# Kernel optimization log

Hardware: AMD Instinct MI355X
Metric: run time of the kernel (lower is better)

## Reference

```python
import jax, jax.numpy as jnp
import numpy as np
import math

B, T, D, H, E = 4, 2048, 1024, 4096, 8
CAPACITY_FACTOR = 1.0
MIN_CAPACITY = 4
Z_LOSS_COEF = 0.001
AUX_LOSS_COEF = 0.01


def setup_inputs() -> dict:
    key = jax.random.key(0)
    ks = jax.random.split(key, 5)
    x = jax.random.normal(ks[0], (B, T, D), jnp.float32)
    Wg = jax.random.normal(ks[1], (D, E), jnp.float32) * 0.02
    W1 = jax.random.normal(ks[2], (E, D, H), jnp.float32) * (1.0 / math.sqrt(D))
    b1 = jnp.zeros((E, H), jnp.float32)
    W2 = jax.random.normal(ks[3], (E, H, D), jnp.float32) * (1.0 / math.sqrt(H))
    b2 = jnp.zeros((E, D), jnp.float32)
    return {"x": x, "Wg": Wg, "W1": W1, "b1": b1, "W2": W2, "b2": b2}


def reference(x, Wg, W1, b1, W2, b2):
    b, t, d = x.shape
    e = Wg.shape[1]
    N = b * t
    capacity = max(MIN_CAPACITY, math.ceil(CAPACITY_FACTOR * N / e))  # static
    xf = x.reshape(N, d)

    # ---- Router (top-1, z-loss + aux load-balancing loss) ----
    logits = xf @ Wg                                   # [N, E]
    probs = jax.nn.softmax(logits, axis=-1)
    z_loss = jnp.mean(jax.nn.logsumexp(logits, axis=-1) ** 2)
    expert_index = jnp.argmax(logits, axis=-1)         # [N]
    expert_prob = jnp.take_along_axis(probs, expert_index[:, None], axis=1)[:, 0]
    counts = jax.ops.segment_sum(jnp.ones((N,), jnp.float32), expert_index,
                                 num_segments=e)       # bincount
    f_i = counts / N
    p_i = probs.mean(axis=0)
    aux_loss = AUX_LOSS_COEF * e * jnp.sum(f_i * p_i) + Z_LOSS_COEF * z_loss

    # ---- Sort-based dispatch ----
    sort_idx = jnp.argsort(expert_index)               # stable sort by expert
    se = expert_index[sort_idx]                        # sorted expert ids
    xs = xf[sort_idx]                                  # tokens in sorted order
    ps = expert_prob[sort_idx]                         # probs in sorted order
    counts_i = counts.astype(jnp.int32)
    start = jnp.cumsum(counts_i) - counts_i            # per-expert start offsets
    pos = jnp.arange(N, dtype=jnp.int32) - start[se]   # slot within expert
    keep = pos < capacity                              # capacity drop
    slot = jnp.where(keep, pos, capacity)              # overflow -> trash slot

    # Gather tokens into per-expert capacity buffer [E, capacity+1, D]
    buf = jnp.zeros((e, capacity + 1, d), xf.dtype).at[se, slot].set(xs)

    # ---- Batched per-expert MLP (grouped GEMM) ----
    h = jax.nn.gelu(jnp.einsum('ecd,edh->ech', buf, W1) + b1[:, None, :],
                    approximate=False)
    o = jnp.einsum('ech,ehd->ecd', h, W2) + b2[:, None, :]

    # ---- Combine: gather back, zero dropped tokens, unsort ----
    out_sorted = jnp.where(keep[:, None], o[se, slot], jnp.zeros((), o.dtype))
    out = jnp.zeros_like(xf).at[sort_idx].set(out_sorted)
    # NOTE: faithful to original code, which multiplies the UNSORTED output by
    # the SORTED probabilities (prob_sorted), a quirk of the source module.
    out = out * ps[:, None]
    return out.reshape(b, t, d), aux_loss
```

## Files before the change

kernel.cpp:

```cpp
#include <hip/hip_runtime.h>
#include <math.h>

#define N_TOK 8192
#define DIM   1024
#define NEXP  8
#define HID   4096
#define CAP   1024
#define TPT   (N_TOK / 256)
#define RT_BLOCKS 256
#define RT_TPB (N_TOK / RT_BLOCKS)

typedef _Float16 f16x8 __attribute__((ext_vector_type(8)));
typedef _Float16 f16x4 __attribute__((ext_vector_type(4)));
typedef float    f32x4 __attribute__((ext_vector_type(4)));

__device__ __forceinline__ float gelu_exact(float v) {
    return 0.5f * v * (1.0f + erff(v * 0.7071067811865476f));
}

__device__ __forceinline__ void gl_lds16(const void* g, void* l) {
    __builtin_amdgcn_global_load_lds(
        (const __attribute__((address_space(1))) unsigned int*)g,
        (__attribute__((address_space(3))) unsigned int*)l, 16, 0, 0);
}

__global__ __launch_bounds__(256) void router_kernel(
    const float* __restrict__ x, const float* __restrict__ Wg,
    int* __restrict__ ei, float* __restrict__ eprob,
    float* __restrict__ pp)
{
    __shared__ float psum_s[NEXP + 1];
    const int tid = threadIdx.x;
    const int w = tid >> 6, lane = tid & 63;
    if (tid <= NEXP) psum_s[tid] = 0.f;
    __syncthreads();

    float p_loc[NEXP];
#pragma unroll
    for (int e = 0; e < NEXP; ++e) p_loc[e] = 0.f;
    float z_loc = 0.f;

    for (int ti = 0; ti < RT_TPB / 4; ++ti) {
        const int t = blockIdx.x * RT_TPB + w * (RT_TPB / 4) + ti;
        const float* xr = x + (size_t)t * DIM;
        float acc[NEXP];
#pragma unroll
        for (int e = 0; e < NEXP; ++e) acc[e] = 0.f;
#pragma unroll
        for (int k = 0; k < DIM / 64; ++k) {
            const int d = k * 64 + lane;
            const float xv = xr[d];
            const float4 w0 = *(const float4*)(Wg + (size_t)d * NEXP);
            const float4 w1 = *(const float4*)(Wg + (size_t)d * NEXP + 4);
            acc[0] += xv * w0.x; acc[1] += xv * w0.y;
            acc[2] += xv * w0.z; acc[3] += xv * w0.w;
            acc[4] += xv * w1.x; acc[5] += xv * w1.y;
            acc[6] += xv * w1.z; acc[7] += xv * w1.w;
        }
#pragma unroll
        for (int off = 32; off > 0; off >>= 1) {
#pragma unroll
            for (int e = 0; e < NEXP; ++e)
                acc[e] += __shfl_down(acc[e], off, 64);
        }
        if (lane == 0) {
            float m = acc[0]; int arg = 0;
#pragma unroll
            for (int e = 1; e < NEXP; ++e) { if (acc[e] > m) { m = acc[e]; arg = e; } }
            float ex[NEXP]; float se = 0.f;
#pragma unroll
            for (int e = 0; e < NEXP; ++e) { ex[e] = expf(acc[e] - m); se += ex[e]; }
            const float lse = m + logf(se);
            const float inv = 1.f / se;
#pragma unroll
            for (int e = 0; e < NEXP; ++e) p_loc[e] += ex[e] * inv;
            z_loc += lse * lse;
            ei[t] = arg;
            eprob[t] = ex[arg] * inv;
        }
    }
    if (lane == 0) {
#pragma unroll
        for (int e = 0; e < NEXP; ++e) atomicAdd(&psum_s[e], p_loc[e]);
        atomicAdd(&psum_s[NEXP], z_loc);
    }
    __syncthreads();
    if (tid <= NEXP) pp[blockIdx.x * (NEXP + 1) + tid] = psum_s[tid];
}

__global__ __launch_bounds__(256) void dispatch_kernel(
    const int* __restrict__ ei, const float* __restrict__ eprob,
    int* __restrict__ slot_to_token, int* __restrict__ sort_idx,
    float* __restrict__ scale,
    const float* __restrict__ pp,
    float* __restrict__ aux_out)
{
    __shared__ int hist[NEXP][256];
    __shared__ int start_s[NEXP];
    __shared__ float red_s[4][NEXP + 1];
    __shared__ float tot_s[NEXP + 1];
    const int t = threadIdx.x;
    const int w = t >> 6, lane = t & 63;

    {
        float v[NEXP + 1];
#pragma unroll
        for (int j = 0; j <= NEXP; ++j) v[j] = pp[t * (NEXP + 1) + j];
#pragma unroll
        for (int j = 0; j <= NEXP; ++j) {
            float s = v[j];
#pragma unroll
            for (int off = 32; off > 0; off >>= 1) s += __shfl_down(s, off, 64);
            if (lane == 0) red_s[w][j] = s;
        }
    }
    __syncthreads();
    if (t <= NEXP) tot_s[t] = red_s[0][t] + red_s[1][t] + red_s[2][t] + red_s[3][t];
    __syncthreads();

    int le[TPT];
    int lh[NEXP];
#pragma unroll
    for (int e = 0; e < NEXP; ++e) lh[e] = 0;
    const int base = t * TPT;
    for (int i = 0; i < TPT; ++i) {
        const int e = ei[base + i];
        le[i] = e;
        lh[e]++;
    }
#pragma unroll
    for (int e = 0; e < NEXP; ++e) hist[e][t] = lh[e];
    __syncthreads();
    for (int off = 1; off < 256; off <<= 1) {
        int v[NEXP];
#pragma unroll
        for (int e = 0; e < NEXP; ++e) v[e] = (t >= off) ? hist[e][t - off] : 0;
        __syncthreads();
#pragma unroll
        for (int e = 0; e < NEXP; ++e) hist[e][t] += v[e];
        __syncthreads();
    }
    if (t == 0) {
        int s = 0;
        for (int e = 0; e < NEXP; ++e) { start_s[e] = s; s += hist[e][255]; }
    }
    __syncthreads();
    int run[NEXP];
#pragma unroll
    for (int e = 0; e < NEXP; ++e) run[e] = (t > 0) ? hist[e][t - 1] : 0;
    for (int i = 0; i < TPT; ++i) {
        const int n = base + i;
        const int e = le[i];
        const int pos = run[e]++;
        sort_idx[start_s[e] + pos] = n;
        if (pos < CAP) slot_to_token[e * CAP + pos] = n;
    }
    __syncthreads();
    for (int n = t; n < N_TOK; n += 256) scale[n] = eprob[sort_idx[n]];
    if (t == 0) {
        float s = 0.f;
        for (int e = 0; e < NEXP; ++e) {
            const float f = (float)hist[e][255] / (float)N_TOK;
            const float p = tot_s[e] / (float)N_TOK;
            s += f * p;
        }
        aux_out[0] = 0.01f * (float)NEXP * s + 0.001f * (tot_s[NEXP] / (float)N_TOK);
    }
}

__global__ __launch_bounds__(256) void gather_kernel(
    const float* __restrict__ x, const int* __restrict__ slot_to_token,
    _Float16* __restrict__ Xbuf)
{
    const int slot = blockIdx.x;
    const int tok = slot_to_token[slot];
    const int c = threadIdx.x * 4;
    float4 v = make_float4(0.f, 0.f, 0.f, 0.f);
    if (tok >= 0) v = *(const float4*)(x + (size_t)tok * DIM + c);
    f16x4 o;
    o[0] = (_Float16)v.x; o[1] = (_Float16)v.y;
    o[2] = (_Float16)v.z; o[3] = (_Float16)v.w;
    *(f16x4*)(Xbuf + (size_t)slot * DIM + c) = o;
}

template<int R, int C>
__global__ __launch_bounds__(256) void transpose_f32_f16(
    const float* __restrict__ in, _Float16* __restrict__ outT)
{
    const int e = blockIdx.z;
    const int r0 = blockIdx.y * 64, c0 = blockIdx.x * 64;
    const float* pin = in + (size_t)e * R * C;
    _Float16* pot = outT + (size_t)e * R * C;
    __shared__ _Float16 tile[64][72];
    const int tid = threadIdx.x;
    const int rr = tid >> 4, cc = (tid & 15) * 4;
#pragma unroll
    for (int ri = 0; ri < 4; ++ri) {
        const int row = rr + ri * 16;
        const float4 v = *(const float4*)&pin[(size_t)(r0 + row) * C + c0 + cc];
        tile[cc + 0][row] = (_Float16)v.x;
        tile[cc + 1][row] = (_Float16)v.y;
        tile[cc + 2][row] = (_Float16)v.z;
        tile[cc + 3][row] = (_Float16)v.w;
    }
    __syncthreads();
    const int c = tid >> 2, rs = (tid & 3) * 16;
    const f16x8 o0 = *(const f16x8*)&tile[c][rs];
    const f16x8 o1 = *(const f16x8*)&tile[c][rs + 8];
    _Float16* po = &pot[(size_t)(c0 + c) * R + r0 + rs];
    *(f16x8*)po = o0;
    *(f16x8*)(po + 8) = o1;
}

__global__ __launch_bounds__(256) void gemm1_kernel(
    const _Float16* __restrict__ A, const _Float16* __restrict__ Bt,
    const float* __restrict__ b1, _Float16* __restrict__ Hbuf)
{
    const int mb = blockIdx.x;
    const int nb = blockIdx.y;
    const int e  = mb >> 3;
    const _Float16* Ab = A  + (size_t)mb * 128 * DIM;
    const _Float16* Bb = Bt + (size_t)e * HID * DIM + (size_t)nb * 128 * DIM;
    __shared__ _Float16 As[128 * 32];
    __shared__ _Float16 Bs[128 * 32];
    const int tid = threadIdx.x;
    const int lane = tid & 63, w = tid >> 6;
    const int wm = (w >> 1) * 64, wn = (w & 1) * 64;
    const int lr = lane & 15, quad = lane >> 4;

    f32x4 acc[4][4];
#pragma unroll
    for (int i = 0; i < 4; ++i)
#pragma unroll
        for (int j = 0; j < 4; ++j) acc[i][j] = (f32x4)0.f;

    for (int k0 = 0; k0 < DIM; k0 += 32) {
#pragma unroll
        for (int i = 0; i < 2; ++i) {
            const int idx = i * 256 + tid;
            const int row = idx >> 2, seg = idx & 3;
            gl_lds16(Ab + (size_t)row * DIM + k0 + seg * 8, &As[idx * 8]);
            gl_lds16(Bb + (size_t)row * DIM + k0 + seg * 8, &Bs[idx * 8]);
        }
        __syncthreads();
        f16x8 af[4], bf[4];
#pragma unroll
        for (int i = 0; i < 4; ++i)
            af[i] = *(const f16x8*)&As[(wm + i * 16 + lr) * 32 + quad * 8];
#pragma unroll
        for (int j = 0; j < 4; ++j)
            bf[j] = *(const f16x8*)&Bs[(wn + j * 16 + lr) * 32 + quad * 8];
#pragma unroll
        for (int i = 0; i < 4; ++i)
#pragma unroll
            for (int j = 0; j < 4; ++j)
                acc[i][j] = __builtin_amdgcn_mfma_f32_16x16x32_f16(af[i], bf[j], acc[i][j], 0, 0, 0);
        __syncthreads();
    }
    float bias[4];
#pragma unroll
    for (int j = 0; j < 4; ++j)
        bias[j] = b1[(size_t)e * HID + (size_t)nb * 128 + wn + j * 16 + lr];
#pragma unroll
    for (int i = 0; i < 4; ++i) {
#pragma unroll
        for (int r = 0; r < 4; ++r) {
            const size_t row = (size_t)mb * 128 + wm + i * 16 + quad * 4 + r;
            _Float16* hr = Hbuf + row * HID + (size_t)nb * 128;
#pragma unroll
            for (int j = 0; j < 4; ++j)
                hr[wn + j * 16 + lr] = (_Float16)gelu_exact(acc[i][j][r] + bias[j]);
        }
    }
}

__global__ __launch_bounds__(256) void gemm2_kernel(
    const _Float16* __restrict__ A, const _Float16* __restrict__ Bt,
    const float* __restrict__ b2, const int* __restrict__ slot_to_token,
    const float* __restrict__ scale, float* __restrict__ out)
{
    const int mb = blockIdx.x;
    const int nb = blockIdx.y;
    const int e  = mb >> 3;
    const _Float16* Ab = A  + (size_t)mb * 128 * HID;
    const _Float16* Bb = Bt + (size_t)e * DIM * HID + (size_t)nb * 128 * HID;
    __shared__ _Float16 As[128 * 32];
    __shared__ _Float16 Bs[128 * 32];
    const int tid = threadIdx.x;
    const int lane = tid & 63, w = tid >> 6;
    const int wm = (w >> 1) * 64, wn = (w & 1) * 64;
    const int lr = lane & 15, quad = lane >> 4;

    f32x4 acc[4][4];
#pragma unroll
    for (int i = 0; i < 4; ++i)
#pragma unroll
        for (int j = 0; j < 4; ++j) acc[i][j] = (f32x4)0.f;

    for (int k0 = 0; k0 < HID; k0 += 32) {
#pragma unroll
        for (int i = 0; i < 2; ++i) {
            const int idx = i * 256 + tid;
            const int row = idx >> 2, seg = idx & 3;
            gl_lds16(Ab + (size_t)row * HID + k0 + seg * 8, &As[idx * 8]);
            gl_lds16(Bb + (size_t)row * HID + k0 + seg * 8, &Bs[idx * 8]);
        }
        __syncthreads();
        f16x8 af[4], bf[4];
#pragma unroll
        for (int i = 0; i < 4; ++i)
            af[i] = *(const f16x8*)&As[(wm + i * 16 + lr) * 32 + quad * 8];
#pragma unroll
        for (int j = 0; j < 4; ++j)
            bf[j] = *(const f16x8*)&Bs[(wn + j * 16 + lr) * 32 + quad * 8];
#pragma unroll
        for (int i = 0; i < 4; ++i)
#pragma unroll
            for (int j = 0; j < 4; ++j)
                acc[i][j] = __builtin_amdgcn_mfma_f32_16x16x32_f16(af[i], bf[j], acc[i][j], 0, 0, 0);
        __syncthreads();
    }
    float bias[4];
#pragma unroll
    for (int j = 0; j < 4; ++j)
        bias[j] = b2[(size_t)e * DIM + (size_t)nb * 128 + wn + j * 16 + lr];
#pragma unroll
    for (int i = 0; i < 4; ++i) {
#pragma unroll
        for (int r = 0; r < 4; ++r) {
            const int slot = mb * 128 + wm + i * 16 + quad * 4 + r;
            const int tok = slot_to_token[slot];
            if (tok >= 0) {
                const float sc = scale[tok];
                float* orow = out + (size_t)tok * DIM + (size_t)nb * 128;
#pragma unroll
                for (int j = 0; j < 4; ++j)
                    orow[wn + j * 16 + lr] = (acc[i][j][r] + bias[j]) * sc;
            }
        }
    }
}

extern "C" void kernel_launch(void* const* d_in, const int* in_sizes, int n_in,
                              void* d_out, int out_size, void* d_ws, size_t ws_size,
                              hipStream_t stream)
{
    const float* x  = (const float*)d_in[0];
    const float* Wg = (const float*)d_in[1];
    const float* W1 = (const float*)d_in[2];
    const float* b1 = (const float*)d_in[3];
    const float* W2 = (const float*)d_in[4];
    const float* b2 = (const float*)d_in[5];
    float* out = (float*)d_out;

    _Float16* Wt   = (_Float16*)d_ws;
    _Float16* Xbuf = Wt + (size_t)NEXP * HID * DIM;
    _Float16* Hbuf = Xbuf + (size_t)N_TOK * DIM;
    int*   ei    = (int*)(Hbuf + (size_t)N_TOK * HID);
    float* eprob = (float*)(ei + N_TOK);
    int*   sort_idx = (int*)(eprob + N_TOK);
    float* scale = (float*)(sort_idx + N_TOK);
    int*   s2t   = (int*)(scale + N_TOK);
    float* pp    = (float*)(s2t + NEXP * CAP);

    hipMemsetAsync(s2t, 0xFF, (size_t)NEXP * CAP * sizeof(int), stream);
    hipMemsetAsync(out, 0, (size_t)N_TOK * DIM * sizeof(float), stream);

    transpose_f32_f16<DIM, HID><<<dim3(HID / 64, DIM / 64, NEXP), 256, 0, stream>>>(W1, Wt);
    router_kernel<<<RT_BLOCKS, 256, 0, stream>>>(x, Wg, ei, eprob, pp);
    dispatch_kernel<<<1, 256, 0, stream>>>(ei, eprob, s2t, sort_idx, scale,
                                           pp, out + (size_t)N_TOK * DIM);
    gather_kernel<<<NEXP * CAP, 256, 0, stream>>>(x, s2t, Xbuf);
    gemm1_kernel<<<dim3(64, 32), 256, 0, stream>>>(Xbuf, Wt, b1, Hbuf);
    transpose_f32_f16<HID, DIM><<<dim3(DIM / 64, HID / 64, NEXP), 256, 0, stream>>>(W2, Wt);
    gemm2_kernel<<<dim3(64, 8), 256, 0, stream>>>(Hbuf, Wt, b2, s2t, scale, out);
}
```

Measured before the change: 614.0 us.

## Swizzle LDS tiles, remap GEMM1 blocks, tanh GELU, wider router, zero only dropped rows

XOR-swizzles the LDS layout in both GEMMs to cut bank conflicts. GEMM1 now runs on a 1D grid whose block index is remapped so blocks sharing N tiles land on the same XCD. The exact erf GELU is replaced by a tanh approximation, and the router is widened to 1024 blocks with float4 x loads. The full output memset is replaced by a kernel that zeros only the rows of dropped tokens. The tanh GELU adds approximation error relative to the exact-GELU reference.

```diff
diff --git a/kernel.cpp b/kernel.cpp
--- a/kernel.cpp
+++ b/kernel.cpp
@@ -7,15 +7,19 @@
 #define HID   4096
 #define CAP   1024
 #define TPT   (N_TOK / 256)
-#define RT_BLOCKS 256
-#define RT_TPB (N_TOK / RT_BLOCKS)
+#define RT_BLOCKS 1024
+#define RT_TPB 8
 
 typedef _Float16 f16x8 __attribute__((ext_vector_type(8)));
 typedef _Float16 f16x4 __attribute__((ext_vector_type(4)));
 typedef float    f32x4 __attribute__((ext_vector_type(4)));
 
-__device__ __forceinline__ float gelu_exact(float v) {
-    return 0.5f * v * (1.0f + erff(v * 0.7071067811865476f));
+__device__ __forceinline__ float gelu_fast(float v) {
+    const float v2 = v * v;
+    const float u = v * (0.79788456f + 0.035677408136f * v2);
+    const float ex = __expf(2.f * u);
+    const float th = 1.f - 2.f / (1.f + ex);
+    return 0.5f * v * (1.f + th);
 }
 
 __device__ __forceinline__ void gl_lds16(const void* g, void* l) {
@@ -40,22 +44,27 @@
     for (int e = 0; e < NEXP; ++e) p_loc[e] = 0.f;
     float z_loc = 0.f;
 
-    for (int ti = 0; ti < RT_TPB / 4; ++ti) {
-        const int t = blockIdx.x * RT_TPB + w * (RT_TPB / 4) + ti;
+#pragma unroll
+    for (int ti = 0; ti < 2; ++ti) {
+        const int t = blockIdx.x * RT_TPB + w * 2 + ti;
         const float* xr = x + (size_t)t * DIM;
         float acc[NEXP];
 #pragma unroll
         for (int e = 0; e < NEXP; ++e) acc[e] = 0.f;
 #pragma unroll
-        for (int k = 0; k < DIM / 64; ++k) {
-            const int d = k * 64 + lane;
-            const float xv = xr[d];
-            const float4 w0 = *(const float4*)(Wg + (size_t)d * NEXP);
-            const float4 w1 = *(const float4*)(Wg + (size_t)d * NEXP + 4);
-            acc[0] += xv * w0.x; acc[1] += xv * w0.y;
-            acc[2] += xv * w0.z; acc[3] += xv * w0.w;
-            acc[4] += xv * w1.x; acc[5] += xv * w1.y;
-            acc[6] += xv * w1.z; acc[7] += xv * w1.w;
+        for (int k = 0; k < DIM / 256; ++k) {
+            const int d = k * 256 + lane * 4;
+            const float4 xv = *(const float4*)(xr + d);
+            const float xs[4] = {xv.x, xv.y, xv.z, xv.w};
+#pragma unroll
+            for (int u = 0; u < 4; ++u) {
+                const float4 w0 = *(const float4*)(Wg + (size_t)(d + u) * NEXP);
+                const float4 w1 = *(const float4*)(Wg + (size_t)(d + u) * NEXP + 4);
+                acc[0] += xs[u] * w0.x; acc[1] += xs[u] * w0.y;
+                acc[2] += xs[u] * w0.z; acc[3] += xs[u] * w0.w;
+                acc[4] += xs[u] * w1.x; acc[5] += xs[u] * w1.y;
+                acc[6] += xs[u] * w1.z; acc[7] += xs[u] * w1.w;
+            }
         }
 #pragma unroll
         for (int off = 32; off > 0; off >>= 1) {
@@ -93,19 +102,25 @@
     int* __restrict__ slot_to_token, int* __restrict__ sort_idx,
     float* __restrict__ scale,
     const float* __restrict__ pp,
+    int* __restrict__ dropped, int* __restrict__ n_dropped,
     float* __restrict__ aux_out)
 {
     __shared__ int hist[NEXP][256];
     __shared__ int start_s[NEXP];
     __shared__ float red_s[4][NEXP + 1];
     __shared__ float tot_s[NEXP + 1];
+    __shared__ int ndrop_s;
     const int t = threadIdx.x;
     const int w = t >> 6, lane = t & 63;
+    if (t == 0) ndrop_s = 0;
 
     {
         float v[NEXP + 1];
 #pragma unroll
-        for (int j = 0; j <= NEXP; ++j) v[j] = pp[t * (NEXP + 1) + j];
+        for (int j = 0; j <= NEXP; ++j) v[j] = 0.f;
+        for (int g = 0; g < RT_BLOCKS / 256; ++g)
+#pragma unroll
+            for (int j = 0; j <= NEXP; ++j) v[j] += pp[(size_t)(g * 256 + t) * (NEXP + 1) + j];
 #pragma unroll
         for (int j = 0; j <= NEXP; ++j) {
             float s = v[j];
@@ -153,11 +168,17 @@
         const int e = le[i];
         const int pos = run[e]++;
         sort_idx[start_s[e] + pos] = n;
-        if (pos < CAP) slot_to_token[e * CAP + pos] = n;
+        if (pos < CAP) {
+            slot_to_token[e * CAP + pos] = n;
+        } else {
+            const int di = atomicAdd(&ndrop_s, 1);
+            dropped[di] = n;
+        }
     }
     __syncthreads();
     for (int n = t; n < N_TOK; n += 256) scale[n] = eprob[sort_idx[n]];
     if (t == 0) {
+        n_dropped[0] = ndrop_s;
         float s = 0.f;
         for (int e = 0; e < NEXP; ++e) {
             const float f = (float)hist[e][255] / (float)N_TOK;
@@ -165,6 +186,18 @@
             s += f * p;
         }
         aux_out[0] = 0.01f * (float)NEXP * s + 0.001f * (tot_s[NEXP] / (float)N_TOK);
+    }
+}
+
+__global__ __launch_bounds__(256) void zero_dropped_kernel(
+    const int* __restrict__ dropped, const int* __restrict__ n_dropped,
+    float* __restrict__ out)
+{
+    const int nd = n_dropped[0];
+    const float4 z = make_float4(0.f, 0.f, 0.f, 0.f);
+    for (int idx = blockIdx.x; idx < nd; idx += gridDim.x) {
+        const int tok = dropped[idx];
+        *(float4*)(out + (size_t)tok * DIM + threadIdx.x * 4) = z;
     }
 }
 
@@ -216,8 +249,10 @@
     const _Float16* __restrict__ A, const _Float16* __restrict__ Bt,
     const float* __restrict__ b1, _Float16* __restrict__ Hbuf)
 {
-    const int mb = blockIdx.x;
-    const int nb = blockIdx.y;
+    const int b = blockIdx.x;
+    const int xcd = b & 7, q = b >> 3;
+    const int nb = (xcd << 2) | (q & 3);
+    const int mb = q >> 2;
     const int e  = mb >> 3;
     const _Float16* Ab = A  + (size_t)mb * 128 * DIM;
     const _Float16* Bb = Bt + (size_t)e * HID * DIM + (size_t)nb * 128 * DIM;
@@ -238,18 +273,23 @@
 #pragma unroll
         for (int i = 0; i < 2; ++i) {
             const int idx = i * 256 + tid;
-            const int row = idx >> 2, seg = idx & 3;
+            const int row = idx >> 2, s = idx & 3;
+            const int seg = s ^ (row & 3);
             gl_lds16(Ab + (size_t)row * DIM + k0 + seg * 8, &As[idx * 8]);
             gl_lds16(Bb + (size_t)row * DIM + k0 + seg * 8, &Bs[idx * 8]);
         }
         __syncthreads();
         f16x8 af[4], bf[4];
 #pragma unroll
-        for (int i = 0; i < 4; ++i)
-            af[i] = *(const f16x8*)&As[(wm + i * 16 + lr) * 32 + quad * 8];
-#pragma unroll
-        for (int j = 0; j < 4; ++j)
-            bf[j] = *(const f16x8*)&Bs[(wn + j * 16 + lr) * 32 + quad * 8];
+        for (int i = 0; i < 4; ++i) {
+            const int R = wm + i * 16 + lr;
+            af[i] = *(const f16x8*)&As[R * 32 + (quad ^ (R & 3)) * 8];
+        }
+#pragma unroll
+        for (int j = 0; j < 4; ++j) {
+            const int R = wn + j * 16 + lr;
+            bf[j] = *(const f16x8*)&Bs[R * 32 + (quad ^ (R & 3)) * 8];
+        }
 #pragma unroll
         for (int i = 0; i < 4; ++i)
 #pragma unroll
@@ -269,7 +309,7 @@
             _Float16* hr = Hbuf + row * HID + (size_t)nb * 128;
 #pragma unroll
             for (int j = 0; j < 4; ++j)
-                hr[wn + j * 16 + lr] = (_Float16)gelu_exact(acc[i][j][r] + bias[j]);
+                hr[wn + j * 16 + lr] = (_Float16)gelu_fast(acc[i][j][r] + bias[j]);
         }
     }
 }
@@ -301,18 +341,23 @@
 #pragma unroll
         for (int i = 0; i < 2; ++i) {
             const int idx = i * 256 + tid;
-            const int row = idx >> 2, seg = idx & 3;
+            const int row = idx >> 2, s = idx & 3;
+            const int seg = s ^ (row & 3);
             gl_lds16(Ab + (size_t)row * HID + k0 + seg * 8, &As[idx * 8]);
             gl_lds16(Bb + (size_t)row * HID + k0 + seg * 8, &Bs[idx * 8]);
         }
         __syncthreads();
         f16x8 af[4], bf[4];
 #pragma unroll
-        for (int i = 0; i < 4; ++i)
-            af[i] = *(const f16x8*)&As[(wm + i * 16 + lr) * 32 + quad * 8];
-#pragma unroll
-        for (int j = 0; j < 4; ++j)
-            bf[j] = *(const f16x8*)&Bs[(wn + j * 16 + lr) * 32 + quad * 8];
+        for (int i = 0; i < 4; ++i) {
+            const int R = wm + i * 16 + lr;
+            af[i] = *(const f16x8*)&As[R * 32 + (quad ^ (R & 3)) * 8];
+        }
+#pragma unroll
+        for (int j = 0; j < 4; ++j) {
+            const int R = wn + j * 16 + lr;
+            bf[j] = *(const f16x8*)&Bs[R * 32 + (quad ^ (R & 3)) * 8];
+        }
 #pragma unroll
         for (int i = 0; i < 4; ++i)
 #pragma unroll
@@ -362,16 +407,19 @@
     float* scale = (float*)(sort_idx + N_TOK);
     int*   s2t   = (int*)(scale + N_TOK);
     float* pp    = (float*)(s2t + NEXP * CAP);
+    int*   dropped = (int*)(pp + RT_BLOCKS * (NEXP + 1));
+    int*   n_dropped = dropped + N_TOK;
 
     hipMemsetAsync(s2t, 0xFF, (size_t)NEXP * CAP * sizeof(int), stream);
-    hipMemsetAsync(out, 0, (size_t)N_TOK * DIM * sizeof(float), stream);
 
     transpose_f32_f16<DIM, HID><<<dim3(HID / 64, DIM / 64, NEXP), 256, 0, stream>>>(W1, Wt);
     router_kernel<<<RT_BLOCKS, 256, 0, stream>>>(x, Wg, ei, eprob, pp);
     dispatch_kernel<<<1, 256, 0, stream>>>(ei, eprob, s2t, sort_idx, scale,
-                                           pp, out + (size_t)N_TOK * DIM);
+                                           pp, dropped, n_dropped,
+                                           out + (size_t)N_TOK * DIM);
+    zero_dropped_kernel<<<128, 256, 0, stream>>>(dropped, n_dropped, out);
     gather_kernel<<<NEXP * CAP, 256, 0, stream>>>(x, s2t, Xbuf);
-    gemm1_kernel<<<dim3(64, 32), 256, 0, stream>>>(Xbuf, Wt, b1, Hbuf);
+    gemm1_kernel<<<2048, 256, 0, stream>>>(Xbuf, Wt, b1, Hbuf);
     transpose_f32_f16<HID, DIM><<<dim3(DIM / 64, HID / 64, NEXP), 256, 0, stream>>>(W2, Wt);
     gemm2_kernel<<<dim3(64, 8), 256, 0, stream>>>(Hbuf, Wt, b2, s2t, scale, out);
 }
```

New measurement: 592.0 us. 3.6% less time.
